# Kernel optimization log

Measured on AMD Instinct MI355X. Metric: run time of the kernel, lower is better.

Reference implementation:

```python
import jax, jax.numpy as jnp
from jax import lax
import numpy as np

N, T, V = 32, 32, 128
C_FEAT, C_BOX, C_CLS = 256, 4, 4
C_IN = C_FEAT + C_BOX + C_CLS  # 264 (is_scene=False concatenates x,b,c)
C_OUT = 64
K = 9
EPS = 1e-3  # keras BatchNormalization default epsilon


def _bn4(x, g, b, m, v):
    # inference-mode BN over channel axis 1 of (N,C,T,V)
    s = (g * lax.rsqrt(v + EPS))[None, :, None, None]
    return (x - m[None, :, None, None]) * s + b[None, :, None, None]


def _stgcn(x, a, imp, w, bw, ga, ba, ma, va, al, wt, bt, gb, bb, mb, vb, residual):
    res = x if residual else 0.0
    # SGCN: 1x1 conv (channels_first) then adjacency aggregation; dropout is identity at inference
    h = jnp.einsum('nctv,co->notv', x, w) + bw[None, :, None, None]
    h = jnp.einsum('nctv,ntvw->nctw', h, a * imp)
    # TGCN: BN -> PReLU(alpha per (C,T,V)) -> temporal conv (K,1) SAME -> BN -> (dropout=id)
    h = _bn4(h, ga, ba, ma, va)
    h = jnp.where(h >= 0, h, al[None] * h)
    h = lax.conv_general_dilated(h, wt, (1, 1), 'SAME',
                                 dimension_numbers=('NCHW', 'HWIO', 'NCHW')) + bt[None, :, None, None]
    h = _bn4(h, gb, bb, mb, vb)
    return h + res  # use_mdn=True -> no final PReLU


def _forward(x, b, c, a, dbn_g, dbn_b, dbn_m, dbn_v,
             w0, bw0, imp0, g0a, b0a, m0a, v0a, al0, wt0, bt0, g0b, b0b, m0b, v0b,
             w1, bw1, imp1, g1a, b1a, m1a, v1a, al1, wt1, bt1, g1b, b1b, m1b, v1b):
    x = jnp.concatenate([x, b, c], axis=-1)  # (N,T,V,C_IN)
    n, t, v, cc = x.shape
    # data BN over flattened (V*C) channel axis, exactly as the TF reshapes do
    x = jnp.transpose(x, (0, 2, 3, 1)).reshape(n, v * cc, t)
    s = (dbn_g * lax.rsqrt(dbn_v + EPS))[None, :, None]
    x = (x - dbn_m[None, :, None]) * s + dbn_b[None, :, None]
    # NOTE: the original does transpose(0,1,3,2) then a *reshape* to (N,C,T,V); replicate exactly
    x = x.reshape(n, v, cc, t).transpose(0, 1, 3, 2).reshape(n, cc, t, v)
    x = _stgcn(x, a, imp0, w0, bw0, g0a, b0a, m0a, v0a, al0, wt0, bt0, g0b, b0b, m0b, v0b, residual=False)
    x = _stgcn(x, a, imp1, w1, bw1, g1a, b1a, m1a, v1a, al1, wt1, bt1, g1b, b1b, m1b, v1b, residual=True)
    x = x[:, :, :, 0]  # (N,C_OUT,T)
    return jnp.transpose(x, (0, 2, 1))  # (N,T,C_OUT)


def setup_inputs():
    key = jax.random.key(0)
    ks = jax.random.split(key, 40)
    rn = lambda k, s, sc=1.0: jax.random.normal(k, s, jnp.float32) * sc
    ru = lambda k, s, lo, hi: jax.random.uniform(k, s, jnp.float32, lo, hi)
    d = {}
    d['x'] = rn(ks[0], (N, T, V, C_FEAT))
    d['b'] = rn(ks[1], (N, T, V, C_BOX))
    d['c'] = ru(ks[2], (N, T, V, C_CLS), 0.0, 1.0)
    d['a'] = ru(ks[3], (N, T, V, V), 0.0, 1.0)
    d['dbn_g'] = ru(ks[4], (V * C_IN,), 0.5, 1.5)
    d['dbn_b'] = rn(ks[5], (V * C_IN,), 0.1)
    d['dbn_m'] = rn(ks[6], (V * C_IN,), 0.1)
    d['dbn_v'] = ru(ks[7], (V * C_IN,), 0.5, 1.5)

    def mk_layer(i, cin, kb):
        d['w%d' % i] = rn(ks[kb], (cin, C_OUT), (1.0 / cin) ** 0.5)
        d['bw%d' % i] = rn(ks[kb + 1], (C_OUT,), 0.01)
        d['imp%d' % i] = rn(ks[kb + 2], (V, V), (2.0 / (V * V)) ** 0.5)
        d['g%da' % i] = ru(ks[kb + 3], (C_OUT,), 0.5, 1.5)
        d['b%da' % i] = rn(ks[kb + 4], (C_OUT,), 0.1)
        d['m%da' % i] = rn(ks[kb + 5], (C_OUT,), 0.1)
        d['v%da' % i] = ru(ks[kb + 6], (C_OUT,), 0.5, 1.5)
        d['al%d' % i] = ru(ks[kb + 7], (C_OUT, T, V), 0.0, 0.3)
        d['wt%d' % i] = rn(ks[kb + 8], (K, 1, C_OUT, C_OUT), (1.0 / (K * C_OUT)) ** 0.5)
        d['bt%d' % i] = rn(ks[kb + 9], (C_OUT,), 0.01)
        d['g%db' % i] = ru(ks[kb + 10], (C_OUT,), 0.5, 1.5)
        d['b%db' % i] = rn(ks[kb + 11], (C_OUT,), 0.1)
        d['m%db' % i] = rn(ks[kb + 12], (C_OUT,), 0.1)
        d['v%db' % i] = ru(ks[kb + 13], (C_OUT,), 0.5, 1.5)

    mk_layer(0, C_IN, 8)
    mk_layer(1, C_OUT, 22)
    return d


def reference(x, b, c, a, dbn_g, dbn_b, dbn_m, dbn_v,
              w0, bw0, imp0, g0a, b0a, m0a, v0a, al0, wt0, bt0, g0b, b0b, m0b, v0b,
              w1, bw1, imp1, g1a, b1a, m1a, v1a, al1, wt1, bt1, g1b, b1b, m1b, v1b):
    return _forward(x, b, c, a, dbn_g, dbn_b, dbn_m, dbn_v,
                    w0, bw0, imp0, g0a, b0a, m0a, v0a, al0, wt0, bt0, g0b, b0b, m0b, v0b,
                    w1, bw1, imp1, g1a, b1a, m1a, v1a, al1, wt1, bt1, g1b, b1b, m1b, v1b)
```

## Files before the change

### kernel.cpp

```cpp
#include <hip/hip_runtime.h>
#include <hip/hip_bf16.h>

typedef unsigned short u16;
typedef unsigned int   u32;

#define N_   32
#define T_   32
#define V_   128
#define CIN_ 264
#define CO_  64
#define KT_  9
#define EPS_ 1e-3f

#define OFF_DBN_S 0
#define OFF_DBN_O 33792
#define OFF_W0    67584
#define OFF_BW0   84480
#define OFF_A0S   84544
#define OFF_A0O   84608
#define OFF_B0S   84672
#define OFF_B0O   84736
#define OFF_W1    84800
#define OFF_BW1   88896
#define OFF_A1S   88960
#define OFF_A1O   89024
#define OFF_B1S   89088
#define OFF_B1O   89152
#define PREP_TOTAL 110464

#define B_P    0
#define B_FLAG 360448
#define B_W0A  360512
#define B_WTA  397440
#define B_H0   524288
#define B_G0   (B_H0 + 16777216)
#define B_L0   (B_G0 + 16777216)
#define B_G1P  (B_L0 + 33554432)
#define B_END  (B_G1P + 262144)

typedef short bf16x8 __attribute__((ext_vector_type(8)));
typedef float f32x4  __attribute__((ext_vector_type(4)));

__device__ __forceinline__ float bf2f(u16 u) { return __uint_as_float(((u32)u) << 16); }
__device__ __forceinline__ u16 f2bf(float f) {
    u32 x = __float_as_uint(f);
    return (u16)((x + 0x7fffu + ((x >> 16) & 1u)) >> 16);
}
__device__ __forceinline__ float ldin(const void* p, u32 i, int f32) {
    return f32 ? ((const float*)p)[i] : bf2f(((const u16*)p)[i]);
}
__device__ __forceinline__ u32 swzv(u32 row) {
    u32 m = (row >> 3) & 7u;
    return (m << 4) ^ ((m & 3u) << 5);
}

__global__ void k_detect(const void* a, int* flag) {
    if (threadIdx.x == 0 && blockIdx.x == 0) {
        const u16* p = (const u16*)a;
        int cnt = 0;
        for (int i = 0; i < 64; ++i) {
            float v = bf2f(p[2 * i]);
            if (v >= 0.f && v <= 1.0f) ++cnt;
        }
        *flag = (cnt >= 56) ? 0 : 1;
    }
}

__global__ void k_prep(const void* dbn_g, const void* dbn_b, const void* dbn_m, const void* dbn_v,
                       const void* w0, const void* bw0,
                       const void* g0a, const void* b0a, const void* m0a, const void* v0a,
                       const void* bt0, const void* g0b, const void* b0b, const void* m0b, const void* v0b,
                       const void* w1, const void* bw1,
                       const void* g1a, const void* b1a, const void* m1a, const void* v1a,
                       const void* bt1, const void* g1b, const void* b1b, const void* m1b, const void* v1b,
                       const void* wt0,
                       float* P, u16* W0A, u16* WTA, const int* flagp)
{
    const int f32 = *flagp;
    int i = blockIdx.x * 256 + threadIdx.x;
    if (i < 33792) {
        float s = ldin(dbn_g, i, f32) * rsqrtf(ldin(dbn_v, i, f32) + EPS_);
        P[OFF_DBN_S + i] = s;
        P[OFF_DBN_O + i] = ldin(dbn_b, i, f32) - ldin(dbn_m, i, f32) * s;
    } else if (i < 50688) { int j = i - 33792; P[OFF_W0 + j] = ldin(w0, j, f32); }
    else if (i < 50752) { int j = i - 50688; P[OFF_BW0 + j] = ldin(bw0, j, f32); }
    else if (i < 50816) { int j = i - 50752;
        float s = ldin(g0a, j, f32) * rsqrtf(ldin(v0a, j, f32) + EPS_);
        P[OFF_A0S + j] = s; P[OFF_A0O + j] = ldin(b0a, j, f32) - ldin(m0a, j, f32) * s;
    } else if (i < 50880) { int j = i - 50816;
        float s = ldin(g0b, j, f32) * rsqrtf(ldin(v0b, j, f32) + EPS_);
        P[OFF_B0S + j] = s; P[OFF_B0O + j] = (ldin(bt0, j, f32) - ldin(m0b, j, f32)) * s + ldin(b0b, j, f32);
    } else if (i < 54976) { int j = i - 50880; P[OFF_W1 + j] = ldin(w1, j, f32); }
    else if (i < 55040) { int j = i - 54976; P[OFF_BW1 + j] = ldin(bw1, j, f32); }
    else if (i < 55104) { int j = i - 55040;
        float s = ldin(g1a, j, f32) * rsqrtf(ldin(v1a, j, f32) + EPS_);
        P[OFF_A1S + j] = s; P[OFF_A1O + j] = ldin(b1a, j, f32) - ldin(m1a, j, f32) * s;
    } else if (i < 55168) { int j = i - 55104;
        float s = ldin(g1b, j, f32) * rsqrtf(ldin(v1b, j, f32) + EPS_);
        P[OFF_B1S + j] = s; P[OFF_B1O + j] = (ldin(bt1, j, f32) - ldin(m1b, j, f32)) * s + ldin(b1b, j, f32);
    } else if (i < 73600) {
        int j = i - 55168; int c = j / 288, ci = j - c * 288;
        float val = (ci < 264) ? ldin(w0, (u32)ci * 64 + c, f32)
                  : ((ci == 264) ? ldin(bw0, c, f32) : 0.f);
        W0A[j] = f2bf(val);
    } else if (i < 110464) {
        int j = i - 73600; int k = j >> 12, rem = j & 4095, o = rem >> 6, ii = rem & 63;
        WTA[j] = f2bf(ldin(wt0, ((u32)(k * 64 + ii)) * 64 + o, f32));
    }
}

__global__ __launch_bounds__(256) void k_pwf(const void* __restrict__ xin, const void* __restrict__ bin,
                                             const void* __restrict__ cin2, const float* __restrict__ P,
                                             const u16* __restrict__ W0Ag, u16* __restrict__ h0,
                                             const int* __restrict__ flagp)
{
    __shared__ __align__(16) u16 tile[288 * 64];
    const int f32 = *flagp;
    const int t2 = blockIdx.x, n = blockIdx.y, vh = blockIdx.z;
    const int tid = threadIdx.x;

    for (int e = tid; e < 192; e += 256) {
        int row = 264 + (e >> 3), chunk = e & 7;
        u32 fill = (row == 264) ? 0x3F803F80u : 0u;
        uint4 z = make_uint4(fill, fill, fill, fill);
        u32 byte = (u32)row * 128u + (((u32)chunk * 16u) ^ swzv((u32)row));
        *(uint4*)((char*)tile + byte) = z;
    }
    for (int e = tid; e < 2112; e += 256) {
        int c2 = e >> 3, vv0 = (e & 7) << 3;
        u32 L = (u32)c2 * 4096u + (u32)(t2 * 128 + vh * 64 + vv0);
        u32 vs = L / 8448u;
        u32 r  = L - vs * 8448u;
        u32 ts = r / 264u;
        u32 cc = r - ts * 264u;
        u32 base = ((u32)n * 32u + ts) * 128u + vs;
        u32 ch = vs * 264u + cc;
        float v8[8];
        if (f32) {
            float4 a0, a1;
            if (cc < 256u) {
                const float* sp = (const float*)xin + (size_t)base * 256u + cc;
                a0 = *(const float4*)sp; a1 = *(const float4*)(sp + 4);
            } else {
                a0 = *(const float4*)((const float*)bin  + (size_t)base * 4u);
                a1 = *(const float4*)((const float*)cin2 + (size_t)base * 4u);
            }
            v8[0] = a0.x; v8[1] = a0.y; v8[2] = a0.z; v8[3] = a0.w;
            v8[4] = a1.x; v8[5] = a1.y; v8[6] = a1.z; v8[7] = a1.w;
        } else {
            __align__(16) u16 up[8];
            if (cc < 256u) {
                *(uint4*)up = *(const uint4*)((const u16*)xin + (size_t)base * 256u + cc);
            } else {
                *(ushort4*)&up[0] = *(const ushort4*)((const u16*)bin  + (size_t)base * 4u);
                *(ushort4*)&up[4] = *(const ushort4*)((const u16*)cin2 + (size_t)base * 4u);
            }
#pragma unroll
            for (int j = 0; j < 8; ++j) v8[j] = bf2f(up[j]);
        }
        const float4 s0 = *(const float4*)&P[OFF_DBN_S + ch];
        const float4 s1 = *(const float4*)&P[OFF_DBN_S + ch + 4];
        const float4 o0 = *(const float4*)&P[OFF_DBN_O + ch];
        const float4 o1 = *(const float4*)&P[OFF_DBN_O + ch + 4];
        __align__(16) u16 pk[8];
        pk[0] = f2bf(fmaf(v8[0], s0.x, o0.x));
        pk[1] = f2bf(fmaf(v8[1], s0.y, o0.y));
        pk[2] = f2bf(fmaf(v8[2], s0.z, o0.z));
        pk[3] = f2bf(fmaf(v8[3], s0.w, o0.w));
        pk[4] = f2bf(fmaf(v8[4], s1.x, o1.x));
        pk[5] = f2bf(fmaf(v8[5], s1.y, o1.y));
        pk[6] = f2bf(fmaf(v8[6], s1.z, o1.z));
        pk[7] = f2bf(fmaf(v8[7], s1.w, o1.w));
        u32 byte = (u32)c2 * 128u + (((u32)vv0 * 2u) ^ swzv((u32)c2));
        *(uint4*)((char*)tile + byte) = *(uint4*)pk;
    }
    __syncthreads();

    const int wv = tid >> 6, lane = tid & 63, l16 = lane & 15, quad = lane >> 4;
    f32x4 acc[4];
#pragma unroll
    for (int i = 0; i < 4; ++i) acc[i] = (f32x4){0.f, 0.f, 0.f, 0.f};

#pragma unroll
    for (int ks = 0; ks < 9; ++ks) {
        const int k0 = ks * 32 + quad * 8;
        const u32 xr = swzv((u32)k0);
        const u32 cb = ((u32)(wv * 16 + l16) * 2u) ^ xr;
        bf16x8 af;
#pragma unroll
        for (int j = 0; j < 8; ++j)
            af[j] = (short)*(const u16*)((const char*)tile + (u32)(k0 + j) * 128u + cb);
#pragma unroll
        for (int ni = 0; ni < 4; ++ni) {
            bf16x8 bf = *(const bf16x8*)&W0Ag[(u32)(ni * 16 + l16) * 288 + k0];
            acc[ni] = __builtin_amdgcn_mfma_f32_16x16x32_bf16(af, bf, acc[ni], 0, 0, 0);
        }
    }
    const int v = vh * 64 + wv * 16 + quad * 4;
#pragma unroll
    for (int ni = 0; ni < 4; ++ni) {
        int c = ni * 16 + l16;
        ushort4 rr; u16* rp = (u16*)&rr;
#pragma unroll
        for (int r = 0; r < 4; ++r) rp[r] = f2bf(acc[ni][r]);
        *(ushort4*)&h0[((u32)(n * 64 + c) * 32 + t2) * 128 + v] = rr;
    }
}

__global__ __launch_bounds__(256) void k_graph0(const void* __restrict__ a, const void* __restrict__ imp0,
                                                const void* __restrict__ al0, const float* __restrict__ P,
                                                const u16* __restrict__ h0, u16* __restrict__ g0,
                                                const int* __restrict__ flagp)
{
    __shared__ __align__(16) u16 tile[128 * 128];
    const int f32 = *flagp;
    const int t = blockIdx.x, n = blockIdx.y;
    const int tid = threadIdx.x;
    const u32 abase = (((u32)n * 32u + (u32)t) * 128u) * 128u;

    for (int e = tid; e < 2048; e += 256) {
        int v = e >> 4, w0 = (e & 15) << 3;
        float vals[8];
        if (f32) {
            const float* ap = (const float*)a + abase + (u32)v * 128u + w0;
            const float* ip = (const float*)imp0 + (u32)v * 128u + w0;
            float4 x0 = *(const float4*)ap, x1 = *(const float4*)(ap + 4);
            float4 i0 = *(const float4*)ip, i1 = *(const float4*)(ip + 4);
            vals[0] = x0.x * i0.x; vals[1] = x0.y * i0.y; vals[2] = x0.z * i0.z; vals[3] = x0.w * i0.w;
            vals[4] = x1.x * i1.x; vals[5] = x1.y * i1.y; vals[6] = x1.z * i1.z; vals[7] = x1.w * i1.w;
        } else {
            uint4 xu = *(const uint4*)((const u16*)a + abase + (u32)v * 128u + w0);
            uint4 iu = *(const uint4*)((const u16*)imp0 + (u32)v * 128u + w0);
            const u16* xp = (const u16*)&xu; const u16* ip = (const u16*)&iu;
#pragma unroll
            for (int j = 0; j < 8; ++j) vals[j] = bf2f(xp[j]) * bf2f(ip[j]);
        }
        __align__(16) u16 pk[8];
#pragma unroll
        for (int j = 0; j < 8; ++j) pk[j] = f2bf(vals[j]);
        u32 byte = (u32)v * 256u + (((u32)w0 * 2u) ^ swzv((u32)v));
        *(uint4*)((char*)tile + byte) = *(uint4*)pk;
    }
    __syncthreads();

    const int wv = tid >> 6, lane = tid & 63, l16 = lane & 15, quad = lane >> 4;
    const int n0w = wv * 32;
    const u16* Hb = h0 + ((u32)n * 2048u + (u32)t) * 128u;

    f32x4 acc[4][2];
#pragma unroll
    for (int mi = 0; mi < 4; ++mi) { acc[mi][0] = (f32x4){0,0,0,0}; acc[mi][1] = (f32x4){0,0,0,0}; }
#pragma unroll
    for (int ks = 0; ks < 4; ++ks) {
        const int k0 = ks * 32 + quad * 8;
        const u32 xr = swzv((u32)k0);
        const u32 wb0 = (u32)(n0w + l16) * 2u;
        const u32 wb1 = (u32)(n0w + 16 + l16) * 2u;
        bf16x8 bf0, bf1;
#pragma unroll
        for (int j = 0; j < 8; ++j) {
            const u32 rb = (u32)(k0 + j) * 256u;
            bf0[j] = (short)*(const u16*)((const char*)tile + rb + (wb0 ^ xr));
            bf1[j] = (short)*(const u16*)((const char*)tile + rb + (wb1 ^ xr));
        }
#pragma unroll
        for (int mi = 0; mi < 4; ++mi) {
            bf16x8 af = *(const bf16x8*)&Hb[(u32)(mi * 16 + l16) * 4096u + k0];
            acc[mi][0] = __builtin_amdgcn_mfma_f32_16x16x32_bf16(af, bf0, acc[mi][0], 0, 0, 0);
            acc[mi][1] = __builtin_amdgcn_mfma_f32_16x16x32_bf16(af, bf1, acc[mi][1], 0, 0, 0);
        }
    }
#pragma unroll
    for (int mi = 0; mi < 4; ++mi) {
        const int c0 = mi * 16 + quad * 4;
        const float4 s4 = *(const float4*)&P[OFF_A0S + c0];
        const float4 o4 = *(const float4*)&P[OFF_A0O + c0];
        const float ss[4] = {s4.x, s4.y, s4.z, s4.w};
        const float oo[4] = {o4.x, o4.y, o4.z, o4.w};
#pragma unroll
        for (int ni = 0; ni < 2; ++ni) {
            const int w = n0w + ni * 16 + l16;
            ushort4 rr; u16* rp = (u16*)&rr;
#pragma unroll
            for (int r = 0; r < 4; ++r) {
                float y = fmaf(acc[mi][ni][r], ss[r], oo[r]);
                float alv = ldin(al0, ((u32)(c0 + r) * 32 + t) * 128 + w, f32);
                rp[r] = f2bf((y >= 0.f) ? y : alv * y);
            }
            *(ushort4*)&g0[((u32)(n * 32 + t) * 128 + w) * 64 + c0] = rr;
        }
    }
}

__global__ __launch_bounds__(256) void k_tconv0(const u16* __restrict__ WTAg, const float* __restrict__ P,
                                                const u16* __restrict__ g0, float* __restrict__ L0)
{
    const int t = blockIdx.x, n = blockIdx.y;
    const int tid = threadIdx.x;
    const int kmin = (t < 4) ? (4 - t) : 0;
    const int kmax = (t > 27) ? (35 - t) : 8;
    const int wv = tid >> 6, lane = tid & 63, l16 = lane & 15, quad = lane >> 4;
    const int n0w = wv * 32;

    f32x4 acc[4][2];
#pragma unroll
    for (int mi = 0; mi < 4; ++mi) { acc[mi][0] = (f32x4){0,0,0,0}; acc[mi][1] = (f32x4){0,0,0,0}; }

    for (int k = kmin; k <= kmax; ++k) {
        const u16* Wb = WTAg + (u32)k * 4096u;
        const u16* Bb = g0 + ((u32)(n * 32 + (t + k - 4)) * 128u) * 64u;
#pragma unroll
        for (int ks = 0; ks < 2; ++ks) {
            const int k0 = ks * 32 + quad * 8;
            bf16x8 bf0 = *(const bf16x8*)&Bb[(u32)(n0w + l16) * 64u + k0];
            bf16x8 bf1 = *(const bf16x8*)&Bb[(u32)(n0w + 16 + l16) * 64u + k0];
#pragma unroll
            for (int mi = 0; mi < 4; ++mi) {
                bf16x8 af = *(const bf16x8*)&Wb[(u32)(mi * 16 + l16) * 64u + k0];
                acc[mi][0] = __builtin_amdgcn_mfma_f32_16x16x32_bf16(af, bf0, acc[mi][0], 0, 0, 0);
                acc[mi][1] = __builtin_amdgcn_mfma_f32_16x16x32_bf16(af, bf1, acc[mi][1], 0, 0, 0);
            }
        }
    }
#pragma unroll
    for (int mi = 0; mi < 4; ++mi) {
        const int ob = mi * 16 + quad * 4;
        const float4 s4 = *(const float4*)&P[OFF_B0S + ob];
        const float4 o4 = *(const float4*)&P[OFF_B0O + ob];
        const float ss[4] = {s4.x, s4.y, s4.z, s4.w};
        const float oo[4] = {o4.x, o4.y, o4.z, o4.w};
#pragma unroll
        for (int ni = 0; ni < 2; ++ni) {
            const int v = n0w + ni * 16 + l16;
#pragma unroll
            for (int r = 0; r < 4; ++r)
                L0[((u32)(n * 64 + ob + r) * 32 + t) * 128 + v] = fmaf(acc[mi][ni][r], ss[r], oo[r]);
        }
    }
}

__global__ __launch_bounds__(256) void k_pw1(const void* __restrict__ a, const void* __restrict__ imp1,
                                             const void* __restrict__ al1, const float* __restrict__ P,
                                             const float* __restrict__ L0, float* __restrict__ g1p,
                                             const int* __restrict__ flagp)
{
    __shared__ float amv[V_];
    __shared__ float xr[CO_];
    __shared__ float Ssh;
    const int f32 = *flagp;
    const int t = blockIdx.x, n = blockIdx.y;
    const int tid = threadIdx.x;

    if (tid < V_) {
        float av = ldin(a, (((u32)n * T_ + t) * V_ + tid) * V_ + 0u, f32)
                 * ldin(imp1, (u32)tid * V_ + 0u, f32);
        amv[tid] = av;
    }
    __syncthreads();
    if (tid < 64) {
        float s = amv[tid] + amv[tid + 64];
#pragma unroll
        for (int m = 1; m < 64; m <<= 1) s += __shfl_xor(s, m);
        if (tid == 0) Ssh = s;
    }
    const int c = tid >> 2, sub = tid & 3;
    const float* Lrow = L0 + (u32)n * (CO_ * T_ * V_) + (u32)c * (T_ * V_) + (u32)t * V_ + sub * 32;
    float p = 0.f;
#pragma unroll
    for (int j = 0; j < 32; j += 4) {
        float4 x = *(const float4*)(Lrow + j);
        float4 m = *(const float4*)&amv[sub * 32 + j];
        p = fmaf(x.x, m.x, p); p = fmaf(x.y, m.y, p);
        p = fmaf(x.z, m.z, p); p = fmaf(x.w, m.w, p);
    }
    p += __shfl_xor(p, 1);
    p += __shfl_xor(p, 2);
    if (sub == 0) xr[c] = p;
    __syncthreads();
    if (tid < CO_) {
        const int o = tid;
        float y = P[OFF_BW1 + o] * Ssh;
        for (int cc = 0; cc < CO_; ++cc)
            y = fmaf(xr[cc], P[OFF_W1 + cc * CO_ + o], y);
        y = fmaf(y, P[OFF_A1S + o], P[OFF_A1O + o]);
        float alv = ldin(al1, ((u32)o * T_ + t) * V_ + 0u, f32);
        y = (y >= 0.f) ? y : alv * y;
        g1p[((u32)n * CO_ + o) * T_ + t] = y;
    }
}

__global__ __launch_bounds__(256) void k_tconv1(const void* __restrict__ wt1, const float* __restrict__ P,
                                                const float* __restrict__ g1p, const float* __restrict__ L0,
                                                void* __restrict__ out, const int* __restrict__ flagp)
{
    __shared__ float gl[CO_][40];
    const int f32 = *flagp;
    const int n = blockIdx.x;
    const int tid = threadIdx.x;
    for (int e = tid; e < 512; e += 256) {
        int i = e >> 3, p = e & 7;
        gl[i][(p < 4) ? p : (p + 32)] = 0.f;
    }
    for (int e = tid; e < 2048; e += 256) {
        int i = e >> 5, tt = e & 31;
        gl[i][tt + 4] = g1p[(u32)n * 2048u + (u32)i * 32u + tt];
    }
    __syncthreads();
    const int o = tid & 63, tq = tid >> 6, t0 = tq * 8;
    float acc[8];
#pragma unroll
    for (int j = 0; j < 8; ++j) acc[j] = 0.f;
    for (int i = 0; i < CO_; ++i) {
        float win[16];
#pragma unroll
        for (int m = 0; m < 16; m += 4) *(float4*)&win[m] = *(const float4*)&gl[i][t0 + m];
#pragma unroll
        for (int k = 0; k < KT_; ++k) {
            float wv = ldin(wt1, ((u32)(k * CO_ + i)) * CO_ + o, f32);
#pragma unroll
            for (int j = 0; j < 8; ++j) acc[j] = fmaf(win[j + k], wv, acc[j]);
        }
    }
    const float s1 = P[OFF_B1S + o], o1 = P[OFF_B1O + o];
#pragma unroll
    for (int j = 0; j < 8; ++j) {
        const int t = t0 + j;
        float y = fmaf(acc[j], s1, o1);
        y += L0[(u32)n * (CO_ * T_ * V_) + (u32)o * (T_ * V_) + (u32)t * V_ + 0];
        const u32 oi = ((u32)n * T_ + t) * CO_ + o;
        if (f32) ((float*)out)[oi] = y;
        else     ((u16*)out)[oi]   = f2bf(y);
    }
}

__global__ void k_fail(u16* out, int nel) {
    int i = blockIdx.x * 256 + threadIdx.x;
    if (i < nel) out[i] = 0x7f80;
}

extern "C" void kernel_launch(void* const* d_in, const int* in_sizes, int n_in,
                              void* d_out, int out_size, void* d_ws, size_t ws_size,
                              hipStream_t stream)
{
    const void* xin  = d_in[0];
    const void* bin  = d_in[1];
    const void* cin2 = d_in[2];
    const void* a    = d_in[3];
    const void* dbn_g = d_in[4];
    const void* dbn_b = d_in[5];
    const void* dbn_m = d_in[6];
    const void* dbn_v = d_in[7];
    const void* w0  = d_in[8];
    const void* bw0 = d_in[9];
    const void* imp0 = d_in[10];
    const void* g0a = d_in[11];
    const void* b0a = d_in[12];
    const void* m0a = d_in[13];
    const void* v0a = d_in[14];
    const void* al0 = d_in[15];
    const void* wt0 = d_in[16];
    const void* bt0 = d_in[17];
    const void* g0b = d_in[18];
    const void* b0b = d_in[19];
    const void* m0b = d_in[20];
    const void* v0b = d_in[21];
    const void* w1  = d_in[22];
    const void* bw1 = d_in[23];
    const void* imp1 = d_in[24];
    const void* g1a = d_in[25];
    const void* b1a = d_in[26];
    const void* m1a = d_in[27];
    const void* v1a = d_in[28];
    const void* al1 = d_in[29];
    const void* wt1 = d_in[30];
    const void* bt1 = d_in[31];
    const void* g1b = d_in[32];
    const void* b1b = d_in[33];
    const void* m1b = d_in[34];
    const void* v1b = d_in[35];

    if (ws_size < (size_t)B_END) {
        k_fail<<<(out_size + 255) / 256, 256, 0, stream>>>((u16*)d_out, out_size);
        return;
    }
    char* w = (char*)d_ws;
    float* P    = (float*)(w + B_P);
    int*   flg  = (int*)(w + B_FLAG);
    u16*   W0A  = (u16*)(w + B_W0A);
    u16*   WTA  = (u16*)(w + B_WTA);
    u16*   h0   = (u16*)(w + B_H0);
    u16*   g0   = (u16*)(w + B_G0);
    float* L0   = (float*)(w + B_L0);
    float* g1p  = (float*)(w + B_G1P);

    k_detect<<<1, 64, 0, stream>>>(a, flg);
    k_prep<<<(PREP_TOTAL + 255) / 256, 256, 0, stream>>>(
        dbn_g, dbn_b, dbn_m, dbn_v, w0, bw0, g0a, b0a, m0a, v0a,
        bt0, g0b, b0b, m0b, v0b, w1, bw1, g1a, b1a, m1a, v1a,
        bt1, g1b, b1b, m1b, v1b, wt0, P, W0A, WTA, flg);

    dim3 grid(T_, N_);
    k_pwf   <<<dim3(T_, N_, 2), 256, 0, stream>>>(xin, bin, cin2, P, W0A, h0, flg);
    k_graph0<<<grid, 256, 0, stream>>>(a, imp0, al0, P, h0, g0, flg);
    k_tconv0<<<grid, 256, 0, stream>>>(WTA, P, g0, L0);
    k_pw1   <<<grid, 256, 0, stream>>>(a, imp1, al1, P, L0, g1p, flg);
    k_tconv1<<<dim3(N_), 256, 0, stream>>>(wt1, P, g1p, L0, d_out, flg);
}
```

Baseline: 487.5 us.

## Shrink LDS footprint in pwf and split graph0 over output columns

k_pwf now stages its 288-row input tile in three 96-row phases, keeping accumulators live across phases, so shared memory per block drops threefold. k_graph0 splits the output w dimension across a new grid z axis, halving its LDS tile and per-wave accumulators while doubling block count. The goal is higher occupancy and more parallelism to hide global load latency. In exchange, pwf gains extra barriers that serialize load and MFMA phases, and graph0 re-reads h0 once per half.

```diff
diff --git a/kernel.cpp b/kernel.cpp
--- a/kernel.cpp
+++ b/kernel.cpp
@@ -114,86 +114,91 @@
                                              const u16* __restrict__ W0Ag, u16* __restrict__ h0,
                                              const int* __restrict__ flagp)
 {
-    __shared__ __align__(16) u16 tile[288 * 64];
+    __shared__ __align__(16) u16 tile[96 * 64];
     const int f32 = *flagp;
     const int t2 = blockIdx.x, n = blockIdx.y, vh = blockIdx.z;
     const int tid = threadIdx.x;
-
-    for (int e = tid; e < 192; e += 256) {
-        int row = 264 + (e >> 3), chunk = e & 7;
-        u32 fill = (row == 264) ? 0x3F803F80u : 0u;
-        uint4 z = make_uint4(fill, fill, fill, fill);
-        u32 byte = (u32)row * 128u + (((u32)chunk * 16u) ^ swzv((u32)row));
-        *(uint4*)((char*)tile + byte) = z;
-    }
-    for (int e = tid; e < 2112; e += 256) {
-        int c2 = e >> 3, vv0 = (e & 7) << 3;
-        u32 L = (u32)c2 * 4096u + (u32)(t2 * 128 + vh * 64 + vv0);
-        u32 vs = L / 8448u;
-        u32 r  = L - vs * 8448u;
-        u32 ts = r / 264u;
-        u32 cc = r - ts * 264u;
-        u32 base = ((u32)n * 32u + ts) * 128u + vs;
-        u32 ch = vs * 264u + cc;
-        float v8[8];
-        if (f32) {
-            float4 a0, a1;
-            if (cc < 256u) {
-                const float* sp = (const float*)xin + (size_t)base * 256u + cc;
-                a0 = *(const float4*)sp; a1 = *(const float4*)(sp + 4);
+    const int wv = tid >> 6, lane = tid & 63, l16 = lane & 15, quad = lane >> 4;
+
+    f32x4 acc[4];
+#pragma unroll
+    for (int i = 0; i < 4; ++i) acc[i] = (f32x4){0.f, 0.f, 0.f, 0.f};
+
+    for (int ph = 0; ph < 3; ++ph) {
+        if (ph) __syncthreads();
+        const int rbase = ph * 96;
+        for (int e = tid; e < 768; e += 256) {
+            int rloc = e >> 3, vv0 = (e & 7) << 3;
+            int c2 = rbase + rloc;
+            __align__(16) u16 pk[8];
+            if (c2 >= 264) {
+                u32 fill = (c2 == 264) ? 0x3F803F80u : 0u;
+                ((u32*)pk)[0] = fill; ((u32*)pk)[1] = fill;
+                ((u32*)pk)[2] = fill; ((u32*)pk)[3] = fill;
             } else {
-                a0 = *(const float4*)((const float*)bin  + (size_t)base * 4u);
-                a1 = *(const float4*)((const float*)cin2 + (size_t)base * 4u);
+                u32 L = (u32)c2 * 4096u + (u32)(t2 * 128 + vh * 64 + vv0);
+                u32 vs = L / 8448u;
+                u32 r  = L - vs * 8448u;
+                u32 ts = r / 264u;
+                u32 cc = r - ts * 264u;
+                u32 base = ((u32)n * 32u + ts) * 128u + vs;
+                u32 ch = vs * 264u + cc;
+                float v8[8];
+                if (f32) {
+                    float4 a0, a1;
+                    if (cc < 256u) {
+                        const float* sp = (const float*)xin + (size_t)base * 256u + cc;
+                        a0 = *(const float4*)sp; a1 = *(const float4*)(sp + 4);
+                    } else {
+                        a0 = *(const float4*)((const float*)bin  + (size_t)base * 4u);
+                        a1 = *(const float4*)((const float*)cin2 + (size_t)base * 4u);
+                    }
+                    v8[0] = a0.x; v8[1] = a0.y; v8[2] = a0.z; v8[3] = a0.w;
+                    v8[4] = a1.x; v8[5] = a1.y; v8[6] = a1.z; v8[7] = a1.w;
+                } else {
+                    __align__(16) u16 up[8];
+                    if (cc < 256u) {
+                        *(uint4*)up = *(const uint4*)((const u16*)xin + (size_t)base * 256u + cc);
+                    } else {
+                        *(ushort4*)&up[0] = *(const ushort4*)((const u16*)bin  + (size_t)base * 4u);
+                        *(ushort4*)&up[4] = *(const ushort4*)((const u16*)cin2 + (size_t)base * 4u);
+                    }
+#pragma unroll
+                    for (int j = 0; j < 8; ++j) v8[j] = bf2f(up[j]);
+                }
+                const float4 s0 = *(const float4*)&P[OFF_DBN_S + ch];
+                const float4 s1 = *(const float4*)&P[OFF_DBN_S + ch + 4];
+                const float4 o0 = *(const float4*)&P[OFF_DBN_O + ch];
+                const float4 o1 = *(const float4*)&P[OFF_DBN_O + ch + 4];
+                pk[0] = f2bf(fmaf(v8[0], s0.x, o0.x));
+                pk[1] = f2bf(fmaf(v8[1], s0.y, o0.y));
+                pk[2] = f2bf(fmaf(v8[2], s0.z, o0.z));
+                pk[3] = f2bf(fmaf(v8[3], s0.w, o0.w));
+                pk[4] = f2bf(fmaf(v8[4], s1.x, o1.x));
+                pk[5] = f2bf(fmaf(v8[5], s1.y, o1.y));
+                pk[6] = f2bf(fmaf(v8[6], s1.z, o1.z));
+                pk[7] = f2bf(fmaf(v8[7], s1.w, o1.w));
             }
-            v8[0] = a0.x; v8[1] = a0.y; v8[2] = a0.z; v8[3] = a0.w;
-            v8[4] = a1.x; v8[5] = a1.y; v8[6] = a1.z; v8[7] = a1.w;
-        } else {
-            __align__(16) u16 up[8];
-            if (cc < 256u) {
-                *(uint4*)up = *(const uint4*)((const u16*)xin + (size_t)base * 256u + cc);
-            } else {
-                *(ushort4*)&up[0] = *(const ushort4*)((const u16*)bin  + (size_t)base * 4u);
-                *(ushort4*)&up[4] = *(const ushort4*)((const u16*)cin2 + (size_t)base * 4u);
+            u32 byte = (u32)rloc * 128u + (((u32)vv0 * 2u) ^ swzv((u32)rloc));
+            *(uint4*)((char*)tile + byte) = *(uint4*)pk;
+        }
+        __syncthreads();
+#pragma unroll
+        for (int ks3 = 0; ks3 < 3; ++ks3) {
+            const int ks  = ph * 3 + ks3;
+            const int k0l = ks3 * 32 + quad * 8;
+            const u32 xr  = swzv((u32)k0l);
+            const u32 cb  = ((u32)(wv * 16 + l16) * 2u) ^ xr;
+            bf16x8 af;
+#pragma unroll
+            for (int j = 0; j < 8; ++j)
+                af[j] = (short)*(const u16*)((const char*)tile + (u32)(k0l + j) * 128u + cb);
+            const int k0 = ks * 32 + quad * 8;
+#pragma unroll
+            for (int ni = 0; ni < 4; ++ni) {
+                bf16x8 bf = *(const bf16x8*)&W0Ag[(u32)(ni * 16 + l16) * 288 + k0];
+                acc[ni] = __builtin_amdgcn_mfma_f32_16x16x32_bf16(af, bf, acc[ni], 0, 0, 0);
             }
-#pragma unroll
-            for (int j = 0; j < 8; ++j) v8[j] = bf2f(up[j]);
-        }
-        const float4 s0 = *(const float4*)&P[OFF_DBN_S + ch];
-        const float4 s1 = *(const float4*)&P[OFF_DBN_S + ch + 4];
-        const float4 o0 = *(const float4*)&P[OFF_DBN_O + ch];
-        const float4 o1 = *(const float4*)&P[OFF_DBN_O + ch + 4];
-        __align__(16) u16 pk[8];
-        pk[0] = f2bf(fmaf(v8[0], s0.x, o0.x));
-        pk[1] = f2bf(fmaf(v8[1], s0.y, o0.y));
-        pk[2] = f2bf(fmaf(v8[2], s0.z, o0.z));
-        pk[3] = f2bf(fmaf(v8[3], s0.w, o0.w));
-        pk[4] = f2bf(fmaf(v8[4], s1.x, o1.x));
-        pk[5] = f2bf(fmaf(v8[5], s1.y, o1.y));
-        pk[6] = f2bf(fmaf(v8[6], s1.z, o1.z));
-        pk[7] = f2bf(fmaf(v8[7], s1.w, o1.w));
-        u32 byte = (u32)c2 * 128u + (((u32)vv0 * 2u) ^ swzv((u32)c2));
-        *(uint4*)((char*)tile + byte) = *(uint4*)pk;
-    }
-    __syncthreads();
-
-    const int wv = tid >> 6, lane = tid & 63, l16 = lane & 15, quad = lane >> 4;
-    f32x4 acc[4];
-#pragma unroll
-    for (int i = 0; i < 4; ++i) acc[i] = (f32x4){0.f, 0.f, 0.f, 0.f};
-
-#pragma unroll
-    for (int ks = 0; ks < 9; ++ks) {
-        const int k0 = ks * 32 + quad * 8;
-        const u32 xr = swzv((u32)k0);
-        const u32 cb = ((u32)(wv * 16 + l16) * 2u) ^ xr;
-        bf16x8 af;
-#pragma unroll
-        for (int j = 0; j < 8; ++j)
-            af[j] = (short)*(const u16*)((const char*)tile + (u32)(k0 + j) * 128u + cb);
-#pragma unroll
-        for (int ni = 0; ni < 4; ++ni) {
-            bf16x8 bf = *(const bf16x8*)&W0Ag[(u32)(ni * 16 + l16) * 288 + k0];
-            acc[ni] = __builtin_amdgcn_mfma_f32_16x16x32_bf16(af, bf, acc[ni], 0, 0, 0);
         }
     }
     const int v = vh * 64 + wv * 16 + quad * 4;
@@ -212,25 +217,27 @@
                                                 const u16* __restrict__ h0, u16* __restrict__ g0,
                                                 const int* __restrict__ flagp)
 {
-    __shared__ __align__(16) u16 tile[128 * 128];
+    __shared__ __align__(16) u16 tile[128 * 64];
     const int f32 = *flagp;
-    const int t = blockIdx.x, n = blockIdx.y;
+    const int t = blockIdx.x, n = blockIdx.y, wh = blockIdx.z;
+    const int w0g = wh * 64;
     const int tid = threadIdx.x;
     const u32 abase = (((u32)n * 32u + (u32)t) * 128u) * 128u;
 
-    for (int e = tid; e < 2048; e += 256) {
-        int v = e >> 4, w0 = (e & 15) << 3;
+    for (int e = tid; e < 1024; e += 256) {
+        int v = e >> 3, wl0 = (e & 7) << 3;
+        int wfull = w0g + wl0;
         float vals[8];
         if (f32) {
-            const float* ap = (const float*)a + abase + (u32)v * 128u + w0;
-            const float* ip = (const float*)imp0 + (u32)v * 128u + w0;
+            const float* ap = (const float*)a + abase + (u32)v * 128u + wfull;
+            const float* ip = (const float*)imp0 + (u32)v * 128u + wfull;
             float4 x0 = *(const float4*)ap, x1 = *(const float4*)(ap + 4);
             float4 i0 = *(const float4*)ip, i1 = *(const float4*)(ip + 4);
             vals[0] = x0.x * i0.x; vals[1] = x0.y * i0.y; vals[2] = x0.z * i0.z; vals[3] = x0.w * i0.w;
             vals[4] = x1.x * i1.x; vals[5] = x1.y * i1.y; vals[6] = x1.z * i1.z; vals[7] = x1.w * i1.w;
         } else {
-            uint4 xu = *(const uint4*)((const u16*)a + abase + (u32)v * 128u + w0);
-            uint4 iu = *(const uint4*)((const u16*)imp0 + (u32)v * 128u + w0);
+            uint4 xu = *(const uint4*)((const u16*)a + abase + (u32)v * 128u + wfull);
+            uint4 iu = *(const uint4*)((const u16*)imp0 + (u32)v * 128u + wfull);
             const u16* xp = (const u16*)&xu; const u16* ip = (const u16*)&iu;
 #pragma unroll
             for (int j = 0; j < 8; ++j) vals[j] = bf2f(xp[j]) * bf2f(ip[j]);
@@ -238,36 +245,31 @@
         __align__(16) u16 pk[8];
 #pragma unroll
         for (int j = 0; j < 8; ++j) pk[j] = f2bf(vals[j]);
-        u32 byte = (u32)v * 256u + (((u32)w0 * 2u) ^ swzv((u32)v));
+        u32 byte = (u32)v * 128u + (((u32)wl0 * 2u) ^ swzv((u32)v));
         *(uint4*)((char*)tile + byte) = *(uint4*)pk;
     }
     __syncthreads();
 
     const int wv = tid >> 6, lane = tid & 63, l16 = lane & 15, quad = lane >> 4;
-    const int n0w = wv * 32;
+    const int n0w = wv * 16;
     const u16* Hb = h0 + ((u32)n * 2048u + (u32)t) * 128u;
 
-    f32x4 acc[4][2];
-#pragma unroll
-    for (int mi = 0; mi < 4; ++mi) { acc[mi][0] = (f32x4){0,0,0,0}; acc[mi][1] = (f32x4){0,0,0,0}; }
+    f32x4 acc[4];
+#pragma unroll
+    for (int mi = 0; mi < 4; ++mi) acc[mi] = (f32x4){0, 0, 0, 0};
 #pragma unroll
     for (int ks = 0; ks < 4; ++ks) {
         const int k0 = ks * 32 + quad * 8;
         const u32 xr = swzv((u32)k0);
-        const u32 wb0 = (u32)(n0w + l16) * 2u;
-        const u32 wb1 = (u32)(n0w + 16 + l16) * 2u;
-        bf16x8 bf0, bf1;
-#pragma unroll
-        for (int j = 0; j < 8; ++j) {
-            const u32 rb = (u32)(k0 + j) * 256u;
-            bf0[j] = (short)*(const u16*)((const char*)tile + rb + (wb0 ^ xr));
-            bf1[j] = (short)*(const u16*)((const char*)tile + rb + (wb1 ^ xr));
-        }
+        const u32 cb = ((u32)(n0w + l16) * 2u) ^ xr;
+        bf16x8 bf;
+#pragma unroll
+        for (int j = 0; j < 8; ++j)
+            bf[j] = (short)*(const u16*)((const char*)tile + (u32)(k0 + j) * 128u + cb);
 #pragma unroll
         for (int mi = 0; mi < 4; ++mi) {
             bf16x8 af = *(const bf16x8*)&Hb[(u32)(mi * 16 + l16) * 4096u + k0];
-            acc[mi][0] = __builtin_amdgcn_mfma_f32_16x16x32_bf16(af, bf0, acc[mi][0], 0, 0, 0);
-            acc[mi][1] = __builtin_amdgcn_mfma_f32_16x16x32_bf16(af, bf1, acc[mi][1], 0, 0, 0);
+            acc[mi] = __builtin_amdgcn_mfma_f32_16x16x32_bf16(af, bf, acc[mi], 0, 0, 0);
         }
     }
 #pragma unroll
@@ -277,18 +279,15 @@
         const float4 o4 = *(const float4*)&P[OFF_A0O + c0];
         const float ss[4] = {s4.x, s4.y, s4.z, s4.w};
         const float oo[4] = {o4.x, o4.y, o4.z, o4.w};
-#pragma unroll
-        for (int ni = 0; ni < 2; ++ni) {
-            const int w = n0w + ni * 16 + l16;
-            ushort4 rr; u16* rp = (u16*)&rr;
-#pragma unroll
-            for (int r = 0; r < 4; ++r) {
-                float y = fmaf(acc[mi][ni][r], ss[r], oo[r]);
-                float alv = ldin(al0, ((u32)(c0 + r) * 32 + t) * 128 + w, f32);
-                rp[r] = f2bf((y >= 0.f) ? y : alv * y);
-            }
-            *(ushort4*)&g0[((u32)(n * 32 + t) * 128 + w) * 64 + c0] = rr;
-        }
+        const int w = w0g + n0w + l16;
+        ushort4 rr; u16* rp = (u16*)&rr;
+#pragma unroll
+        for (int r = 0; r < 4; ++r) {
+            float y = fmaf(acc[mi][r], ss[r], oo[r]);
+            float alv = ldin(al0, ((u32)(c0 + r) * 32 + t) * 128 + w, f32);
+            rp[r] = f2bf((y >= 0.f) ? y : alv * y);
+        }
+        *(ushort4*)&g0[((u32)(n * 32 + t) * 128 + w) * 64 + c0] = rr;
     }
 }
 
@@ -501,7 +500,7 @@
 
     dim3 grid(T_, N_);
     k_pwf   <<<dim3(T_, N_, 2), 256, 0, stream>>>(xin, bin, cin2, P, W0A, h0, flg);
-    k_graph0<<<grid, 256, 0, stream>>>(a, imp0, al0, P, h0, g0, flg);
+    k_graph0<<<dim3(T_, N_, 2), 256, 0, stream>>>(a, imp0, al0, P, h0, g0, flg);
     k_tconv0<<<grid, 256, 0, stream>>>(WTA, P, g0, L0);
     k_pw1   <<<grid, 256, 0, stream>>>(a, imp1, al1, P, L0, g1p, flg);
     k_tconv1<<<dim3(N_), 256, 0, stream>>>(wt1, P, g1p, L0, d_out, flg);
```

Measured after the change: 508.0 us. 4.2% more time.
